# Optimization experiments

Measured on AMD Instinct MI355X. Metric: run time of the kernel, lower is better.

The kernel has to match this reference:

```python
import jax, jax.numpy as jnp
import numpy as np
from jax import lax

EPS = 1e-10
N_MOMENTS = 10


def setup_inputs() -> dict:
    key = jax.random.key(0)
    y = jax.random.normal(key, (8192, 16384), dtype=jnp.float32)
    return {"y": y}


def reference(y):
    # y: [B, L]
    L = y.shape[-1]
    mean = jnp.mean(y, axis=-1)                      # [B]
    z = y - mean[:, None]                            # [B, L] centered values
    # torch.std uses the unbiased estimator (ddof=1)
    std = jnp.sqrt(jnp.sum(z * z, axis=-1) / (L - 1)) + EPS  # [B]

    # moment 0: signed log of |mean| (not clamped, per original)
    m0 = jnp.sign(mean) * jnp.log(jnp.abs(mean) + EPS)       # [B]

    # higher central moments via a single running-power scan over orders 2..N
    def step(zp, _):
        zp = zp * z                                  # z**p
        return zp, jnp.mean(zp, axis=-1)             # E[(y-mean)**p], [B]

    _, cms = lax.scan(step, z, None, length=N_MOMENTS - 1)   # [N-1, B]

    powers = jnp.arange(2, N_MOMENTS + 1, dtype=y.dtype)[:, None]  # [N-1, 1]
    norm = cms / (std[None, :] ** powers + EPS)               # normalized moments
    mj = jnp.clip(jnp.sign(norm) * jnp.log(jnp.abs(norm) + EPS), -10.0, 10.0)

    return jnp.concatenate([m0[:, None], mj.T], axis=1)       # [B, N_MOMENTS]
```

## Files before the change

### kernel.cpp

```cpp
#include <hip/hip_runtime.h>
#include <math.h>

#define ROWLEN 16384
#define BLOCK  256
#define NCHUNK 16
#define NWAVE  (BLOCK / 64)
#define NMOM   9
#define EPSV   1e-10

typedef float f32x2 __attribute__((ext_vector_type(2)));

__device__ __forceinline__ f32x2 pk_mul(f32x2 a, f32x2 b)
{
    f32x2 d;
    asm("v_pk_mul_f32 %0, %1, %2" : "=v"(d) : "v"(a), "v"(b));
    return d;
}

__global__ __launch_bounds__(BLOCK, 5) void moments_kernel(
    const float* __restrict__ y, float* __restrict__ out)
{
    const int row  = blockIdx.x;
    const int tid  = threadIdx.x;
    const int wave = tid >> 6;
    const int lane = tid & 63;

    const float4* yrow = reinterpret_cast<const float4*>(y + (size_t)row * ROWLEN);

    float4 v[NCHUNK];
#pragma unroll
    for (int i = 0; i < NCHUNK; ++i)
        v[i] = yrow[i * BLOCK + tid];

    double tsum = 0.0;
#pragma unroll
    for (int i = 0; i < NCHUNK; ++i) {
        float s = (v[i].x + v[i].y) + (v[i].z + v[i].w);
        tsum += (double)s;
    }
#pragma unroll
    for (int off = 32; off > 0; off >>= 1)
        tsum += __shfl_xor(tsum, off, 64);

    __shared__ double wsum[NWAVE];
    if (lane == 0) wsum[wave] = tsum;
    __syncthreads();

    double total = 0.0;
#pragma unroll
    for (int w = 0; w < NWAVE; ++w) total += wsum[w];

    const double meand = total * (1.0 / (double)ROWLEN);
    const float  meanf = (float)meand;

    double acc[NMOM];
#pragma unroll
    for (int p = 0; p < NMOM; ++p) acc[p] = 0.0;

#pragma unroll
    for (int i = 0; i < NCHUNK; ++i) {
        const float4 c = v[i];
        const f32x2 za = { c.x - meanf, c.y - meanf };
        const f32x2 zb = { c.z - meanf, c.w - meanf };
        f32x2 pa = pk_mul(za, za);
        f32x2 pb = pk_mul(zb, zb);
        acc[0] += (double)((pa.x + pa.y) + (pb.x + pb.y));
#pragma unroll
        for (int p = 1; p < NMOM; ++p) {
            pa = pk_mul(pa, za);
            pb = pk_mul(pb, zb);
            acc[p] += (double)((pa.x + pa.y) + (pb.x + pb.y));
        }
    }

#pragma unroll
    for (int p = 0; p < NMOM; ++p) {
#pragma unroll
        for (int off = 32; off > 0; off >>= 1)
            acc[p] += __shfl_xor(acc[p], off, 64);
    }

    __shared__ double wacc[NWAVE][NMOM];
    if (lane == 0) {
#pragma unroll
        for (int p = 0; p < NMOM; ++p) wacc[wave][p] = acc[p];
    }
    __syncthreads();

    if (tid < 10) {
        const double N = (double)ROWLEN;
        float* o = out + (size_t)row * 10;

        double s2 = 0.0;
#pragma unroll
        for (int w = 0; w < NWAVE; ++w) s2 += wacc[w][0];
        const double stdv = sqrt(s2 / (N - 1.0)) + EPSV;

        if (tid == 0) {
            const double sg0 = (meand > 0.0) ? 1.0 : (meand < 0.0 ? -1.0 : 0.0);
            o[0] = (float)sg0 * logf((float)(fabs(meand) + EPSV));
        } else {
            const int p = tid - 1;
            double s = 0.0;
#pragma unroll
            for (int w = 0; w < NWAVE; ++w) s += wacc[w][p];

            double sp = stdv;
            for (int k = 0; k <= p; ++k) sp *= stdv;

            const double cm  = s / N;
            const double nrm = cm / (sp + EPSV);
            const double sg  = (nrm > 0.0) ? 1.0 : (nrm < 0.0 ? -1.0 : 0.0);
            float mj = (float)sg * logf((float)(fabs(nrm) + EPSV));
            mj = fminf(10.0f, fmaxf(-10.0f, mj));
            o[tid] = mj;
        }
    }
}

extern "C" void kernel_launch(void* const* d_in, const int* in_sizes, int n_in,
                              void* d_out, int out_size, void* d_ws, size_t ws_size,
                              hipStream_t stream)
{
    const float* y = (const float*)d_in[0];
    float* out = (float*)d_out;
    const int B = in_sizes[0] / ROWLEN;
    moments_kernel<<<B, BLOCK, 0, stream>>>(y, out);
}
```

Baseline: 108.2 us.

## Stream rows through LDS with async global-to-LDS loads, 16 rows per block

```diff
diff --git a/kernel.cpp b/kernel.cpp
--- a/kernel.cpp
+++ b/kernel.cpp
@@ -2,11 +2,13 @@
 #include <math.h>
 
 #define ROWLEN 16384
-#define BLOCK  256
-#define NCHUNK 16
+#define BLOCK  512
+#define NCHUNK 8
 #define NWAVE  (BLOCK / 64)
 #define NMOM   9
 #define EPSV   1e-10
+#define RPB    16
+#define NBLOCKS (8192 / RPB)
 
 typedef float f32x2 __attribute__((ext_vector_type(2)));
 
@@ -17,103 +19,139 @@
     return d;
 }
 
-__global__ __launch_bounds__(BLOCK, 5) void moments_kernel(
+__device__ __forceinline__ void sync_lds()
+{
+    asm volatile("s_waitcnt lgkmcnt(0)" ::: "memory");
+    __builtin_amdgcn_s_barrier();
+    asm volatile("" ::: "memory");
+}
+
+__device__ __forceinline__ void gload_lds16(const float* gsrc, float* ldst)
+{
+    __builtin_amdgcn_global_load_lds(
+        (const __attribute__((address_space(1))) void*)gsrc,
+        (__attribute__((address_space(3))) void*)ldst, 16, 0, 0);
+}
+
+__global__ __launch_bounds__(BLOCK, 4) void moments_kernel(
     const float* __restrict__ y, float* __restrict__ out)
 {
-    const int row  = blockIdx.x;
     const int tid  = threadIdx.x;
     const int wave = tid >> 6;
     const int lane = tid & 63;
+    const int row0 = blockIdx.x * RPB;
 
-    const float4* yrow = reinterpret_cast<const float4*>(y + (size_t)row * ROWLEN);
+    __shared__ float buf[ROWLEN];
+    __shared__ double wsum[NWAVE];
+    __shared__ double wacc[NWAVE][NMOM];
 
-    float4 v[NCHUNK];
+    auto issue = [&](int row) {
+        const float* src = y + (size_t)row * ROWLEN;
+        const int stripe = wave * (ROWLEN / NWAVE);
 #pragma unroll
-    for (int i = 0; i < NCHUNK; ++i)
-        v[i] = yrow[i * BLOCK + tid];
+        for (int i = 0; i < 8; ++i) {
+            const int off = stripe + i * 256;
+            gload_lds16(src + off + lane * 4, buf + off);
+        }
+    };
 
-    double tsum = 0.0;
+    issue(row0);
+
+#pragma unroll 1
+    for (int r = 0; r < RPB; ++r) {
+        const int row = row0 + r;
+
+        asm volatile("s_waitcnt vmcnt(0)" ::: "memory");
+        __builtin_amdgcn_s_barrier();
+        asm volatile("" ::: "memory");
+
+        float4 v[NCHUNK];
+        const float4* b4 = reinterpret_cast<const float4*>(buf);
 #pragma unroll
-    for (int i = 0; i < NCHUNK; ++i) {
-        float s = (v[i].x + v[i].y) + (v[i].z + v[i].w);
-        tsum += (double)s;
-    }
+        for (int i = 0; i < NCHUNK; ++i)
+            v[i] = b4[i * BLOCK + tid];
+        sync_lds();
+
+        if (r + 1 < RPB) issue(row + 1);
+
+        double tsum = 0.0;
 #pragma unroll
-    for (int off = 32; off > 0; off >>= 1)
-        tsum += __shfl_xor(tsum, off, 64);
+        for (int i = 0; i < NCHUNK; ++i) {
+            float s = (v[i].x + v[i].y) + (v[i].z + v[i].w);
+            tsum += (double)s;
+        }
+#pragma unroll
+        for (int off = 32; off > 0; off >>= 1)
+            tsum += __shfl_xor(tsum, off, 64);
+        if (lane == 0) wsum[wave] = tsum;
+        sync_lds();
 
-    __shared__ double wsum[NWAVE];
-    if (lane == 0) wsum[wave] = tsum;
-    __syncthreads();
+        double total = 0.0;
+#pragma unroll
+        for (int w = 0; w < NWAVE; ++w) total += wsum[w];
+        const double meand = total * (1.0 / (double)ROWLEN);
+        const float  meanf = (float)meand;
 
-    double total = 0.0;
+        double acc[NMOM];
 #pragma unroll
-    for (int w = 0; w < NWAVE; ++w) total += wsum[w];
-
-    const double meand = total * (1.0 / (double)ROWLEN);
-    const float  meanf = (float)meand;
-
-    double acc[NMOM];
-#pragma unroll
-    for (int p = 0; p < NMOM; ++p) acc[p] = 0.0;
+        for (int p = 0; p < NMOM; ++p) acc[p] = 0.0;
 
 #pragma unroll
-    for (int i = 0; i < NCHUNK; ++i) {
-        const float4 c = v[i];
-        const f32x2 za = { c.x - meanf, c.y - meanf };
-        const f32x2 zb = { c.z - meanf, c.w - meanf };
-        f32x2 pa = pk_mul(za, za);
-        f32x2 pb = pk_mul(zb, zb);
-        acc[0] += (double)((pa.x + pa.y) + (pb.x + pb.y));
+        for (int i = 0; i < NCHUNK; ++i) {
+            const float4 c = v[i];
+            const f32x2 za = { c.x - meanf, c.y - meanf };
+            const f32x2 zb = { c.z - meanf, c.w - meanf };
+            f32x2 pa = pk_mul(za, za);
+            f32x2 pb = pk_mul(zb, zb);
+            acc[0] += (double)((pa.x + pa.y) + (pb.x + pb.y));
 #pragma unroll
-        for (int p = 1; p < NMOM; ++p) {
-            pa = pk_mul(pa, za);
-            pb = pk_mul(pb, zb);
-            acc[p] += (double)((pa.x + pa.y) + (pb.x + pb.y));
+            for (int p = 1; p < NMOM; ++p) {
+                pa = pk_mul(pa, za);
+                pb = pk_mul(pb, zb);
+                acc[p] += (double)((pa.x + pa.y) + (pb.x + pb.y));
+            }
         }
-    }
 
 #pragma unroll
-    for (int p = 0; p < NMOM; ++p) {
+        for (int p = 0; p < NMOM; ++p) {
 #pragma unroll
-        for (int off = 32; off > 0; off >>= 1)
-            acc[p] += __shfl_xor(acc[p], off, 64);
-    }
+            for (int off = 32; off > 0; off >>= 1)
+                acc[p] += __shfl_xor(acc[p], off, 64);
+        }
+        if (lane == 0) {
+#pragma unroll
+            for (int p = 0; p < NMOM; ++p) wacc[wave][p] = acc[p];
+        }
+        sync_lds();
 
-    __shared__ double wacc[NWAVE][NMOM];
-    if (lane == 0) {
+        if (tid < 10) {
+            const double N = (double)ROWLEN;
+            float* o = out + (size_t)row * 10;
+
+            double s2 = 0.0;
 #pragma unroll
-        for (int p = 0; p < NMOM; ++p) wacc[wave][p] = acc[p];
-    }
-    __syncthreads();
+            for (int w = 0; w < NWAVE; ++w) s2 += wacc[w][0];
+            const double stdv = sqrt(s2 / (N - 1.0)) + EPSV;
 
-    if (tid < 10) {
-        const double N = (double)ROWLEN;
-        float* o = out + (size_t)row * 10;
+            if (tid == 0) {
+                const double sg0 = (meand > 0.0) ? 1.0 : (meand < 0.0 ? -1.0 : 0.0);
+                o[0] = (float)sg0 * logf((float)(fabs(meand) + EPSV));
+            } else {
+                const int p = tid - 1;
+                double s = 0.0;
+#pragma unroll
+                for (int w = 0; w < NWAVE; ++w) s += wacc[w][p];
 
-        double s2 = 0.0;
-#pragma unroll
-        for (int w = 0; w < NWAVE; ++w) s2 += wacc[w][0];
-        const double stdv = sqrt(s2 / (N - 1.0)) + EPSV;
+                double sp = stdv;
+                for (int k = 0; k <= p; ++k) sp *= stdv;
 
-        if (tid == 0) {
-            const double sg0 = (meand > 0.0) ? 1.0 : (meand < 0.0 ? -1.0 : 0.0);
-            o[0] = (float)sg0 * logf((float)(fabs(meand) + EPSV));
-        } else {
-            const int p = tid - 1;
-            double s = 0.0;
-#pragma unroll
-            for (int w = 0; w < NWAVE; ++w) s += wacc[w][p];
-
-            double sp = stdv;
-            for (int k = 0; k <= p; ++k) sp *= stdv;
-
-            const double cm  = s / N;
-            const double nrm = cm / (sp + EPSV);
-            const double sg  = (nrm > 0.0) ? 1.0 : (nrm < 0.0 ? -1.0 : 0.0);
-            float mj = (float)sg * logf((float)(fabs(nrm) + EPSV));
-            mj = fminf(10.0f, fmaxf(-10.0f, mj));
-            o[tid] = mj;
+                const double cm  = s / N;
+                const double nrm = cm / (sp + EPSV);
+                const double sg  = (nrm > 0.0) ? 1.0 : (nrm < 0.0 ? -1.0 : 0.0);
+                float mj = (float)sg * logf((float)(fabs(nrm) + EPSV));
+                mj = fminf(10.0f, fmaxf(-10.0f, mj));
+                o[tid] = mj;
+            }
         }
     }
 }
@@ -125,5 +163,5 @@
     const float* y = (const float*)d_in[0];
     float* out = (float*)d_out;
     const int B = in_sizes[0] / ROWLEN;
-    moments_kernel<<<B, BLOCK, 0, stream>>>(y, out);
+    moments_kernel<<<B / RPB, BLOCK, 0, stream>>>(y, out);
 }
```

Measured after the change: 166.7 us. 54.0% more time.
